# Optimization experiments

Hardware: AMD Instinct MI355X
Metric: run time of the kernel (lower is better)

Reference implementation:

```python
import jax, jax.numpy as jnp
import numpy as np

N, NX, NQ, NU = 262144, 64, 64, 16
STD = 0.5


def setup_inputs() -> dict:
    key = jax.random.key(0)
    ks = jax.random.split(key, 8)
    x = jax.random.normal(ks[0], (N, NX), jnp.float32)
    u = jax.random.normal(ks[1], (N, NU), jnp.float32)
    A = jax.random.normal(ks[2], (NX, NX), jnp.float32) * STD
    B1 = jax.random.normal(ks[3], (NX, NQ), jnp.float32) * STD
    B2 = jax.random.normal(ks[4], (NX, NU), jnp.float32) * STD
    C1 = jax.random.normal(ks[5], (NQ, NX), jnp.float32) * STD
    # D11 is strictly lower triangular (forward substitution / triangular solve)
    D11 = jnp.tril(jax.random.normal(ks[6], (NQ, NQ), jnp.float32) * STD, -1)
    D12 = jax.random.normal(ks[7], (NQ, NU), jnp.float32) * STD
    bv = jnp.zeros((NQ,), jnp.float32)  # bias=False in original module
    bx = jnp.zeros((NX,), jnp.float32)
    return {"x": x, "u": u, "A": A, "B1": B1, "B2": B2,
            "C1": C1, "D11": D11, "D12": D12, "bv": bv, "bx": bx}


def _calculate_w(x, u, C1, D11, D12, bv):
    """Solve w = act(C1 x + D11 w + D12 u + bv) by forward substitution.
    D11 is strictly lower triangular, so row i of w only depends on rows < i."""
    act = jax.nn.relu
    nq = D11.shape[0]
    base = x @ C1.T + u @ D12.T + bv          # (N, nq): input-dependent part
    eye = jnp.eye(nq, dtype=x.dtype)           # one-hot rows for the scatter

    def step(w, inp):
        d_row, b_col, e = inp                  # (nq,), (N,), (nq,)
        v = b_col + w @ d_row                  # (N,)  uses only already-filled w cols
        w = w + act(v)[:, None] * e            # write column i (matches torch select_w)
        return w, None

    w0 = jnp.zeros((x.shape[0], nq), x.dtype)
    w, _ = jax.lax.scan(step, w0, (D11, base.T, eye))
    return w


def reference(x, u, A, B1, B2, C1, D11, D12, bv, bx):
    # x_dot = A x + B1 w + B2 u + bx
    w = _calculate_w(x, u, C1, D11, D12, bv)
    x_dot = x @ A.T + w @ B1.T + u @ B2.T + bx
    return x_dot
```

## Files before the change

### kernel.cpp

```cpp
#include <hip/hip_runtime.h>
#include <utility>

#define NROWS 262144
#define BT 512
#define RPB 128

typedef float f16v __attribute__((ext_vector_type(16)));
typedef float f4v  __attribute__((ext_vector_type(4)));


__global__ void prep_kernel(const float* __restrict__ A, const float* __restrict__ B1,
                            const float* __restrict__ B2, const float* __restrict__ C1,
                            const float* __restrict__ D11, const float* __restrict__ D12,
                            const float* __restrict__ bv, const float* __restrict__ bx,
                            float* __restrict__ ws) {
    int g = blockIdx.x * 256 + threadIdx.x;
    if (g < 4096) {
        int r = g >> 6, c = g & 63;
        int to = c * 64 + r;
        ws[0     + to] = C1[g];
        ws[4096  + to] = D11[g];
        ws[9280  + to] = A[g];
        ws[13376 + to] = B1[g];
    }
    if (g < 1024) {
        int r = g >> 4, c = g & 15;
        int to = c * 64 + r;
        ws[8192  + to] = D12[g];
        ws[17472 + to] = B2[g];
    }
    if (g < 64) {
        ws[9216  + g] = bv[g];
        ws[18496 + g] = bx[g];
    }
}

__device__ __forceinline__ f16v lds16(const float* p) { return *(const f16v*)p; }

template<int Q>
__device__ __forceinline__ float qbcast(float v) {
    return __int_as_float(__builtin_amdgcn_update_dpp(
        0, __float_as_int(v), Q * 0x55, 0xF, 0xF, true));
}

template<int I>
__device__ __forceinline__ void substep(f16v& s, const float* D11s, int c16, int c) {
    const float wv = fmaxf(qbcast<(I >> 4)>(s[I & 15]), 0.0f);
    s += lds16(D11s + I * 64 + c16) * wv;
    s[I & 15] = (c == (I >> 4)) ? wv : s[I & 15];
}

template<int... Is>
__device__ __forceinline__ void subst_all(f16v& s, const float* D11s, int c16, int c,
                                          std::integer_sequence<int, Is...>) {
    (substep<Is>(s, D11s, c16, c), ...);
}

template<int J>
__device__ __forceinline__ void mv64step(f16v& a, const float* Ms, int c16, const f16v& f) {
    a += lds16(Ms + J * 64 + c16) * qbcast<(J >> 4)>(f[J & 15]);
}
template<int... Js>
__device__ __forceinline__ void mv64(f16v& a, const float* Ms, int c16, const f16v& f,
                                     std::integer_sequence<int, Js...>) {
    (mv64step<Js>(a, Ms, c16, f), ...);
}

template<int J>
__device__ __forceinline__ void mv16step(f16v& a, const float* Ms, int c16, const f4v& f) {
    a += lds16(Ms + J * 64 + c16) * qbcast<(J >> 2)>(f[J & 3]);
}
template<int... Js>
__device__ __forceinline__ void mv16(f16v& a, const float* Ms, int c16, const f4v& f,
                                     std::integer_sequence<int, Js...>) {
    (mv16step<Js>(a, Ms, c16, f), ...);
}

__global__ __launch_bounds__(BT, 2) void renl2_fused(const float* __restrict__ x,
                                                     const float* __restrict__ u,
                                                     const float* __restrict__ ws,
                                                     float* __restrict__ out) {
    __shared__ __align__(64) float sm[18560];
    const int tid = threadIdx.x;
    const int c   = tid & 3;
    const int c16 = c << 4;
    const size_t row0 = (size_t)blockIdx.x * RPB;

    const f16v xf = *(const f16v*)(x + row0 * 64 + (size_t)tid * 16);
    const f4v  uf = *(const f4v*) (u + row0 * 16 + (size_t)tid * 4);

    const float4* wsv = (const float4*)ws;
    float4* smv = (float4*)sm;
#pragma unroll
    for (int i = 0; i < 9; i++) smv[tid + i * BT] = wsv[tid + i * BT];
    if (tid < 4640 - 9 * BT) smv[tid + 9 * BT] = wsv[tid + 9 * BT];
    __syncthreads();

    f16v s = lds16(sm + 9216 + c16);
    mv64(s, sm + 0,    c16, xf, std::make_integer_sequence<int, 64>{});
    mv16(s, sm + 8192, c16, uf, std::make_integer_sequence<int, 16>{});

    subst_all(s, sm + 4096, c16, c, std::make_integer_sequence<int, 64>{});

    f16v acc = lds16(sm + 18496 + c16);
    mv64(acc, sm + 13376, c16, s,  std::make_integer_sequence<int, 64>{});
    mv64(acc, sm + 9280,  c16, xf, std::make_integer_sequence<int, 64>{});
    mv16(acc, sm + 17472, c16, uf, std::make_integer_sequence<int, 16>{});

    *(f16v*)(out + (row0 + (size_t)(tid >> 2)) * 64 + c16) = acc;
}

extern "C" void kernel_launch(void* const* d_in, const int* in_sizes, int n_in,
                              void* d_out, int out_size, void* d_ws, size_t ws_size,
                              hipStream_t stream) {
    const float* x   = (const float*)d_in[0];
    const float* u   = (const float*)d_in[1];
    const float* A   = (const float*)d_in[2];
    const float* B1  = (const float*)d_in[3];
    const float* B2  = (const float*)d_in[4];
    const float* C1  = (const float*)d_in[5];
    const float* D11 = (const float*)d_in[6];
    const float* D12 = (const float*)d_in[7];
    const float* bv  = (const float*)d_in[8];
    const float* bx  = (const float*)d_in[9];
    float* out = (float*)d_out;
    float* ws  = (float*)d_ws;

    prep_kernel<<<16, 256, 0, stream>>>(A, B1, B2, C1, D11, D12, bv, bx, ws);
    renl2_fused<<<NROWS / RPB, BT, 0, stream>>>(x, u, ws, out);
}
```

Before: 282.5 us.

## Split rows across 8 lanes with 4 rows per thread and staged weights

Each row is now spread across 8 lanes holding 8 outputs each, with every thread processing 4 rows. Each shared-memory weight load is therefore reused across 4 rows, and cross-lane broadcast uses ds_swizzle instead of quad DPP. The weights are loaded into shared memory in two halves, so the LDS footprint is halved and 3 blocks per CU are allowed. x and u are reloaded from global memory after the substitution rather than kept in registers, and scheduling barriers are inserted. The cost is extra global reloads, an extra block-wide sync, and a longer serial dependency chain per thread.

```diff
diff --git a/kernel.cpp b/kernel.cpp
--- a/kernel.cpp
+++ b/kernel.cpp
@@ -3,10 +3,10 @@
 
 #define NROWS 262144
 #define BT 512
-#define RPB 128
-
-typedef float f16v __attribute__((ext_vector_type(16)));
-typedef float f4v  __attribute__((ext_vector_type(4)));
+#define RPB 256
+
+typedef float f8v __attribute__((ext_vector_type(8)));
+typedef float f2v __attribute__((ext_vector_type(2)));
 
 
 __global__ void prep_kernel(const float* __restrict__ A, const float* __restrict__ B1,
@@ -35,79 +35,152 @@
     }
 }
 
-__device__ __forceinline__ f16v lds16(const float* p) { return *(const f16v*)p; }
-
-template<int Q>
-__device__ __forceinline__ float qbcast(float v) {
-    return __int_as_float(__builtin_amdgcn_update_dpp(
-        0, __float_as_int(v), Q * 0x55, 0xF, 0xF, true));
+__device__ __forceinline__ f8v lds8(const float* p) { return *(const f8v*)p; }
+
+__device__ __forceinline__ void fence_sched() { __builtin_amdgcn_sched_barrier(0); }
+
+template<int O>
+__device__ __forceinline__ float obcast(float v) {
+    return __int_as_float(__builtin_amdgcn_ds_swizzle(
+        __float_as_int(v), (O << 5) | 0x18));
 }
 
 template<int I>
-__device__ __forceinline__ void substep(f16v& s, const float* D11s, int c16, int c) {
-    const float wv = fmaxf(qbcast<(I >> 4)>(s[I & 15]), 0.0f);
-    s += lds16(D11s + I * 64 + c16) * wv;
-    s[I & 15] = (c == (I >> 4)) ? wv : s[I & 15];
-}
-
+__device__ __forceinline__ void substep4(f8v& s0, f8v& s1, f8v& s2, f8v& s3,
+                                         const float* D11s, int c8, int c) {
+    const float w0 = fmaxf(obcast<(I >> 3)>(s0[I & 7]), 0.0f);
+    const float w1 = fmaxf(obcast<(I >> 3)>(s1[I & 7]), 0.0f);
+    const float w2 = fmaxf(obcast<(I >> 3)>(s2[I & 7]), 0.0f);
+    const float w3 = fmaxf(obcast<(I >> 3)>(s3[I & 7]), 0.0f);
+    const f8v m = lds8(D11s + I * 64 + c8);
+    s0 += m * w0;  s1 += m * w1;  s2 += m * w2;  s3 += m * w3;
+    s0[I & 7] = (c == (I >> 3)) ? w0 : s0[I & 7];
+    s1[I & 7] = (c == (I >> 3)) ? w1 : s1[I & 7];
+    s2[I & 7] = (c == (I >> 3)) ? w2 : s2[I & 7];
+    s3[I & 7] = (c == (I >> 3)) ? w3 : s3[I & 7];
+}
 template<int... Is>
-__device__ __forceinline__ void subst_all(f16v& s, const float* D11s, int c16, int c,
-                                          std::integer_sequence<int, Is...>) {
-    (substep<Is>(s, D11s, c16, c), ...);
+__device__ __forceinline__ void subst_all4(f8v& s0, f8v& s1, f8v& s2, f8v& s3,
+                                           const float* D11s, int c8, int c,
+                                           std::integer_sequence<int, Is...>) {
+    (substep4<Is>(s0, s1, s2, s3, D11s, c8, c), ...);
 }
 
 template<int J>
-__device__ __forceinline__ void mv64step(f16v& a, const float* Ms, int c16, const f16v& f) {
-    a += lds16(Ms + J * 64 + c16) * qbcast<(J >> 4)>(f[J & 15]);
+__device__ __forceinline__ void mv64step4(f8v& a0, f8v& a1, f8v& a2, f8v& a3,
+                                          const float* Ms, int c8,
+                                          const f8v& f0, const f8v& f1,
+                                          const f8v& f2, const f8v& f3) {
+    const f8v m = lds8(Ms + J * 64 + c8);
+    a0 += m * obcast<(J >> 3)>(f0[J & 7]);
+    a1 += m * obcast<(J >> 3)>(f1[J & 7]);
+    a2 += m * obcast<(J >> 3)>(f2[J & 7]);
+    a3 += m * obcast<(J >> 3)>(f3[J & 7]);
 }
 template<int... Js>
-__device__ __forceinline__ void mv64(f16v& a, const float* Ms, int c16, const f16v& f,
-                                     std::integer_sequence<int, Js...>) {
-    (mv64step<Js>(a, Ms, c16, f), ...);
+__device__ __forceinline__ void mv64_4(f8v& a0, f8v& a1, f8v& a2, f8v& a3,
+                                       const float* Ms, int c8,
+                                       const f8v& f0, const f8v& f1,
+                                       const f8v& f2, const f8v& f3,
+                                       std::integer_sequence<int, Js...>) {
+    (mv64step4<Js>(a0, a1, a2, a3, Ms, c8, f0, f1, f2, f3), ...);
 }
 
 template<int J>
-__device__ __forceinline__ void mv16step(f16v& a, const float* Ms, int c16, const f4v& f) {
-    a += lds16(Ms + J * 64 + c16) * qbcast<(J >> 2)>(f[J & 3]);
+__device__ __forceinline__ void mv16step4(f8v& a0, f8v& a1, f8v& a2, f8v& a3,
+                                          const float* Ms, int c8,
+                                          const f2v& f0, const f2v& f1,
+                                          const f2v& f2, const f2v& f3) {
+    const f8v m = lds8(Ms + J * 64 + c8);
+    a0 += m * obcast<(J >> 1)>(f0[J & 1]);
+    a1 += m * obcast<(J >> 1)>(f1[J & 1]);
+    a2 += m * obcast<(J >> 1)>(f2[J & 1]);
+    a3 += m * obcast<(J >> 1)>(f3[J & 1]);
 }
 template<int... Js>
-__device__ __forceinline__ void mv16(f16v& a, const float* Ms, int c16, const f4v& f,
-                                     std::integer_sequence<int, Js...>) {
-    (mv16step<Js>(a, Ms, c16, f), ...);
-}
-
-__global__ __launch_bounds__(BT, 2) void renl2_fused(const float* __restrict__ x,
+__device__ __forceinline__ void mv16_4(f8v& a0, f8v& a1, f8v& a2, f8v& a3,
+                                       const float* Ms, int c8,
+                                       const f2v& f0, const f2v& f1,
+                                       const f2v& f2, const f2v& f3,
+                                       std::integer_sequence<int, Js...>) {
+    (mv16step4<Js>(a0, a1, a2, a3, Ms, c8, f0, f1, f2, f3), ...);
+}
+
+__global__ __launch_bounds__(BT, 3) void renl2_fused(const float* __restrict__ x,
                                                      const float* __restrict__ u,
                                                      const float* __restrict__ ws,
                                                      float* __restrict__ out) {
-    __shared__ __align__(64) float sm[18560];
+    __shared__ __align__(64) float sm[9280];
     const int tid = threadIdx.x;
-    const int c   = tid & 3;
-    const int c16 = c << 4;
+    const int c   = tid & 7;
+    const int c8  = c << 3;
+    const int oct = tid >> 3;
     const size_t row0 = (size_t)blockIdx.x * RPB;
 
-    const f16v xf = *(const f16v*)(x + row0 * 64 + (size_t)tid * 16);
-    const f4v  uf = *(const f4v*) (u + row0 * 16 + (size_t)tid * 4);
+    const float* xb = x + (row0 + oct) * 64 + c8;
+    const float* ub = u + (row0 + oct) * 16 + (c << 1);
+    const f8v xf0 = *(const f8v*)(xb);
+    const f8v xf1 = *(const f8v*)(xb + 64 * 64);
+    const f8v xf2 = *(const f8v*)(xb + 128 * 64);
+    const f8v xf3 = *(const f8v*)(xb + 192 * 64);
+    const f2v uf0 = *(const f2v*)(ub);
+    const f2v uf1 = *(const f2v*)(ub + 64 * 16);
+    const f2v uf2 = *(const f2v*)(ub + 128 * 16);
+    const f2v uf3 = *(const f2v*)(ub + 192 * 16);
 
     const float4* wsv = (const float4*)ws;
     float4* smv = (float4*)sm;
 #pragma unroll
-    for (int i = 0; i < 9; i++) smv[tid + i * BT] = wsv[tid + i * BT];
-    if (tid < 4640 - 9 * BT) smv[tid + 9 * BT] = wsv[tid + 9 * BT];
+    for (int i = 0; i < 4; i++) smv[tid + i * BT] = wsv[tid + i * BT];
+    if (tid < 2320 - 4 * BT) smv[tid + 4 * BT] = wsv[tid + 4 * BT];
     __syncthreads();
 
-    f16v s = lds16(sm + 9216 + c16);
-    mv64(s, sm + 0,    c16, xf, std::make_integer_sequence<int, 64>{});
-    mv16(s, sm + 8192, c16, uf, std::make_integer_sequence<int, 16>{});
-
-    subst_all(s, sm + 4096, c16, c, std::make_integer_sequence<int, 64>{});
-
-    f16v acc = lds16(sm + 18496 + c16);
-    mv64(acc, sm + 13376, c16, s,  std::make_integer_sequence<int, 64>{});
-    mv64(acc, sm + 9280,  c16, xf, std::make_integer_sequence<int, 64>{});
-    mv16(acc, sm + 17472, c16, uf, std::make_integer_sequence<int, 16>{});
-
-    *(f16v*)(out + (row0 + (size_t)(tid >> 2)) * 64 + c16) = acc;
+    f8v s0 = lds8(sm + 9216 + c8);
+    f8v s1 = s0, s2 = s0, s3 = s0;
+    mv64_4(s0, s1, s2, s3, sm + 0,    c8, xf0, xf1, xf2, xf3,
+           std::make_integer_sequence<int, 64>{});
+    mv16_4(s0, s1, s2, s3, sm + 8192, c8, uf0, uf1, uf2, uf3,
+           std::make_integer_sequence<int, 16>{});
+    fence_sched();
+
+    subst_all4(s0, s1, s2, s3, sm + 4096, c8, c,
+               std::make_integer_sequence<int, 64>{});
+    fence_sched();
+
+    __syncthreads();
+#pragma unroll
+    for (int i = 0; i < 4; i++) smv[tid + i * BT] = wsv[2320 + tid + i * BT];
+    if (tid < 2320 - 4 * BT) smv[tid + 4 * BT] = wsv[2320 + tid + 4 * BT];
+    __syncthreads();
+
+    f8v acc0 = lds8(sm + 9216 + c8);
+    f8v acc1 = acc0, acc2 = acc0, acc3 = acc0;
+    mv64_4(acc0, acc1, acc2, acc3, sm + 4096, c8, s0, s1, s2, s3,
+           std::make_integer_sequence<int, 64>{});
+    fence_sched();
+
+    size_t r0 = row0;
+    asm volatile("" : "+s"(r0));
+    const float* xb2 = x + (r0 + oct) * 64 + c8;
+    const float* ub2 = u + (r0 + oct) * 16 + (c << 1);
+    const f8v xg0 = *(const f8v*)(xb2);
+    const f8v xg1 = *(const f8v*)(xb2 + 64 * 64);
+    const f8v xg2 = *(const f8v*)(xb2 + 128 * 64);
+    const f8v xg3 = *(const f8v*)(xb2 + 192 * 64);
+    const f2v ug0 = *(const f2v*)(ub2);
+    const f2v ug1 = *(const f2v*)(ub2 + 64 * 16);
+    const f2v ug2 = *(const f2v*)(ub2 + 128 * 16);
+    const f2v ug3 = *(const f2v*)(ub2 + 192 * 16);
+    mv64_4(acc0, acc1, acc2, acc3, sm + 0,    c8, xg0, xg1, xg2, xg3,
+           std::make_integer_sequence<int, 64>{});
+    mv16_4(acc0, acc1, acc2, acc3, sm + 8192, c8, ug0, ug1, ug2, ug3,
+           std::make_integer_sequence<int, 16>{});
+
+    float* ob = out + (row0 + oct) * 64 + c8;
+    *(f8v*)(ob)            = acc0;
+    *(f8v*)(ob + 64 * 64)  = acc1;
+    *(f8v*)(ob + 128 * 64) = acc2;
+    *(f8v*)(ob + 192 * 64) = acc3;
 }
 
 extern "C" void kernel_launch(void* const* d_in, const int* in_sizes, int n_in,
```

Measured after the change: 246.2 us. 1.15x faster.
